# Performance work log

Measured on AMD Instinct MI355X. Metric: run time of the kernel, lower is better.

## Reference

```python
import jax, jax.numpy as jnp
import numpy as np

WIDTH = 1024
HEADS = 16
INIT_SCALE = 0.02


def setup_inputs() -> dict:
    key = jax.random.key(0)
    ks = jax.random.split(key, 5)
    x = jax.random.normal(ks[0], (2, 2048, WIDTH), dtype=jnp.float32)
    # torch Linear weight [out, in]; we store transposed [in, out] for x @ W
    W_qkv = jax.random.normal(ks[1], (WIDTH, 3 * WIDTH), dtype=jnp.float32) * INIT_SCALE
    b_qkv = jnp.zeros((3 * WIDTH,), dtype=jnp.float32)
    W_proj = jax.random.normal(ks[2], (WIDTH, WIDTH), dtype=jnp.float32) * INIT_SCALE
    b_proj = jnp.zeros((WIDTH,), dtype=jnp.float32)
    return {"x": x, "W_qkv": W_qkv, "b_qkv": b_qkv, "W_proj": W_proj, "b_proj": b_proj}


def reference(x, W_qkv, b_qkv, W_proj, b_proj):
    bs, n_ctx, width = x.shape
    heads = HEADS
    attn_ch = width // heads  # per-head channel dim (width*3 // heads // 3)
    scale = 1.0 / np.sqrt(np.sqrt(attn_ch))  # applied to both q and k

    qkv = x @ W_qkv + b_qkv                      # [b, t, 3*width]
    qkv = qkv.reshape(bs, n_ctx, heads, 3 * attn_ch)
    q, k, v = jnp.split(qkv, 3, axis=-1)         # each [b, t, h, c]

    weight = jnp.einsum('bthc,bshc->bhts', q * scale, k * scale)
    wdtype = weight.dtype
    weight = jax.nn.softmax(weight.astype(jnp.float32), axis=-1).astype(wdtype)

    out = jnp.einsum('bhts,bshc->bthc', weight, v).reshape(bs, n_ctx, width)
    return out @ W_proj + b_proj
```

## Files before the change

### kernel.cpp

```cpp
#include <hip/hip_runtime.h>

typedef __attribute__((ext_vector_type(4))) float fx4;
typedef __attribute__((ext_vector_type(16))) float f32x16;
typedef __attribute__((ext_vector_type(8))) short s16x8;
typedef __attribute__((ext_vector_type(2))) unsigned int u32x2;

#define QK_SCALE 0.35355339059327373f
#define LOG2E    1.4426950408889634f

__device__ __forceinline__ short f2bf(float f) {
  union { float f; unsigned int u; } v; v.f = f;
  unsigned int r = v.u + 0x7fffu + ((v.u >> 16) & 1u);
  return (short)(r >> 16);
}

__device__ __forceinline__ unsigned f2u(float f) {
  union { float f; unsigned u; } v; v.f = f; return v.u;
}
__device__ __forceinline__ float u2f(unsigned u) {
  union { unsigned u; float f; } v; v.u = u; return v.f;
}
__device__ __forceinline__ float bf2f(short s) {
  return u2f(((unsigned)(unsigned short)s) << 16);
}

__device__ __forceinline__ float xhalf_max(float x) {
  u32x2 r = __builtin_amdgcn_permlane32_swap(f2u(x), f2u(x), false, false);
  return fmaxf(u2f(r[0]), u2f(r[1]));
}
__device__ __forceinline__ float xhalf_sum(float x) {
  u32x2 r = __builtin_amdgcn_permlane32_swap(f2u(x), f2u(x), false, false);
  return u2f(r[0]) + u2f(r[1]);
}

__device__ __forceinline__ int swz(int row, int cb) {
  return (row * 128 + cb) ^ ((row & 7) << 4);
}

#define GLL(g, lds) __builtin_amdgcn_global_load_lds( \
    (__attribute__((address_space(1))) void*)(void*)(g), \
    (__attribute__((address_space(3))) void*)(void*)(lds), 16, 0, 0)

__global__ __launch_bounds__(256) void prep(
    const float* __restrict__ x, short* __restrict__ x16,
    const float* __restrict__ Wqkv, short* __restrict__ WqkvT,
    const float* __restrict__ Wproj, short* __restrict__ WprojT) {
  const int b = blockIdx.x;
  if (b < 4096) {
    int i = b * 256 + threadIdx.x;
    float4 v = reinterpret_cast<const float4*>(x)[i];
    short4 o;
    o.x = f2bf(v.x); o.y = f2bf(v.y); o.z = f2bf(v.z); o.w = f2bf(v.w);
    reinterpret_cast<short4*>(x16)[i] = o;
    return;
  }
  __shared__ float tile[32][33];
  const float* W; short* WT; int N, bx, by;
  if (b < 7168) { W = Wqkv; WT = WqkvT; N = 3072; int r = b - 4096; bx = r % 96; by = r / 96; }
  else          { W = Wproj; WT = WprojT; N = 1024; int r = b - 7168; bx = r % 32; by = r / 32; }
  const int K = 1024;
  int tx = threadIdx.x & 31, ty = threadIdx.x >> 5;
  int n0 = bx * 32, k0 = by * 32;
#pragma unroll
  for (int i = 0; i < 32; i += 8)
    tile[ty + i][tx] = W[(size_t)(k0 + ty + i) * N + n0 + tx];
  __syncthreads();
#pragma unroll
  for (int i = 0; i < 32; i += 8)
    WT[(size_t)(n0 + ty + i) * K + k0 + tx] = f2bf(tile[tx][ty + i]);
}

template <int MODE>
__global__ __launch_bounds__(256) void gemm_bf16(
    const short* __restrict__ A, const short* __restrict__ Bt,
    const float* __restrict__ bias, float* __restrict__ Cout,
    short* __restrict__ Qo, short* __restrict__ Ko, short* __restrict__ Vo,
    int M, int N, int K) {
  __shared__ __align__(16) char sA[2][128 * 64 * 2];
  __shared__ __align__(16) char sB[2][128 * 64 * 2];
  const int tid = threadIdx.x;
  const int w = tid >> 6, l = tid & 63;
  const int lr = l & 15, lg = l >> 4;
  const int bid = blockIdx.x;
  const int m0 = ((bid & 7) * 4 + ((bid >> 3) & 3)) * 128;
  const int n0 = (bid >> 5) * 128;
  const int wr = (w >> 1) * 64, wc = (w & 1) * 64;

  fx4 accT[4][4] = {};

#pragma unroll
  for (int i = 0; i < 4; ++i) {
    int c = i * 256 + tid;
    int r = c >> 3, p = c & 7;
    int lch = p ^ (r & 7);
    GLL(A + (size_t)(m0 + r) * K + lch * 8, sA[0] + c * 16);
    GLL(Bt + (size_t)(n0 + r) * K + lch * 8, sB[0] + c * 16);
  }
  __syncthreads();

  const int NIT = K >> 6;
  int cur = 0;
  for (int it = 0; it < NIT; ++it) {
    if (it + 1 < NIT) {
      int kt = (it + 1) * 64;
#pragma unroll
      for (int i = 0; i < 4; ++i) {
        int c = i * 256 + tid;
        int r = c >> 3, p = c & 7;
        int lch = p ^ (r & 7);
        GLL(A + (size_t)(m0 + r) * K + kt + lch * 8, sA[cur ^ 1] + c * 16);
        GLL(Bt + (size_t)(n0 + r) * K + kt + lch * 8, sB[cur ^ 1] + c * 16);
      }
    }
#pragma unroll
    for (int kk = 0; kk < 2; ++kk) {
      s16x8 av[4], bv[4];
#pragma unroll
      for (int m = 0; m < 4; ++m)
        av[m] = *reinterpret_cast<const s16x8*>(sA[cur] + swz(wr + m * 16 + lr, kk * 64 + lg * 16));
#pragma unroll
      for (int n = 0; n < 4; ++n)
        bv[n] = *reinterpret_cast<const s16x8*>(sB[cur] + swz(wc + n * 16 + lr, kk * 64 + lg * 16));
#pragma unroll
      for (int n = 0; n < 4; ++n)
#pragma unroll
        for (int m = 0; m < 4; ++m)
          accT[n][m] = __builtin_amdgcn_mfma_f32_16x16x32_bf16(bv[n], av[m], accT[n][m], 0, 0, 0);
    }
    __syncthreads();
    cur ^= 1;
  }

#pragma unroll
  for (int n = 0; n < 4; ++n) {
    const int col0 = n0 + wc + n * 16 + lg * 4;
    const float4 bs = *reinterpret_cast<const float4*>(bias + col0);
    if (MODE == 1) {
#pragma unroll
      for (int m = 0; m < 4; ++m) {
        int row = m0 + wr + m * 16 + lr;
        float4 v;
        v.x = accT[n][m][0] + bs.x; v.y = accT[n][m][1] + bs.y;
        v.z = accT[n][m][2] + bs.z; v.w = accT[n][m][3] + bs.w;
        *reinterpret_cast<float4*>(Cout + (size_t)row * N + col0) = v;
      }
    } else {
      const int h = col0 / 192;
      const int rr = col0 - h * 192;
#pragma unroll
      for (int m = 0; m < 4; ++m) {
        int row = m0 + wr + m * 16 + lr;
        int b = row >> 11, t = row & 2047;
        size_t bh = (size_t)b * 16 + h;
        float v0 = accT[n][m][0] + bs.x, v1 = accT[n][m][1] + bs.y;
        float v2 = accT[n][m][2] + bs.z, v3 = accT[n][m][3] + bs.w;
        if (rr < 64) {
          short4 s4;
          s4.x = f2bf(v0 * (QK_SCALE * LOG2E)); s4.y = f2bf(v1 * (QK_SCALE * LOG2E));
          s4.z = f2bf(v2 * (QK_SCALE * LOG2E)); s4.w = f2bf(v3 * (QK_SCALE * LOG2E));
          *reinterpret_cast<short4*>(Qo + (bh * 2048 + t) * 64 + rr) = s4;
        } else if (rr < 128) {
          short4 s4;
          s4.x = f2bf(v0 * QK_SCALE); s4.y = f2bf(v1 * QK_SCALE);
          s4.z = f2bf(v2 * QK_SCALE); s4.w = f2bf(v3 * QK_SCALE);
          *reinterpret_cast<short4*>(Ko + (bh * 2048 + t) * 64 + (rr - 64)) = s4;
        } else {
          Vo[(bh * 64 + (rr - 128) + 0) * 2048 + t] = f2bf(v0);
          Vo[(bh * 64 + (rr - 128) + 1) * 2048 + t] = f2bf(v1);
          Vo[(bh * 64 + (rr - 128) + 2) * 2048 + t] = f2bf(v2);
          Vo[(bh * 64 + (rr - 128) + 3) * 2048 + t] = f2bf(v3);
        }
      }
    }
  }
}

__global__ __launch_bounds__(256, 4) void attn_fwd(
    const short* __restrict__ Q, const short* __restrict__ Kc,
    const short* __restrict__ VT, short* __restrict__ OW,
    float2* __restrict__ ML) {
  __shared__ __align__(16) char sK[2][8192];
  __shared__ __align__(16) char sV[2][8192];
  const int tid = threadIdx.x;
  const int w = tid >> 6, l = tid & 63;
  const int l31 = l & 31, hi = l >> 5;
  const int bid = blockIdx.x;
  const int bh = (bid & 7) * 4 + ((bid >> 3) & 3);
  const int rest = bid >> 5;
  const int qt = rest >> 1, half = rest & 1;
  const int q0 = qt * 128 + w * 32;
  const int sbase = half * 1024;

  s16x8 qf[4];
  const short* qp = Q + ((size_t)bh * 2048 + q0 + l31) * 64 + hi * 8;
#pragma unroll
  for (int ks = 0; ks < 4; ++ks)
    qf[ks] = *reinterpret_cast<const s16x8*>(qp + ks * 16);

  float m = -1e30f, lsum = 0.f;
  f32x16 o0 = {}, o1 = {};

#pragma unroll
  for (int i = 0; i < 2; ++i) {
    int c = i * 256 + tid, r = c >> 3, pch = c & 7, lch = pch ^ (r & 7);
    GLL(Kc + ((size_t)bh * 2048 + sbase + r) * 64 + lch * 8, sK[0] + c * 16);
    GLL(VT + ((size_t)bh * 64 + r) * 2048 + sbase + lch * 8, sV[0] + c * 16);
  }
  __syncthreads();

  for (int sb = 0; sb < 16; ++sb) {
    const int s0 = sbase + sb * 64;
    if (sb < 15) {
#pragma unroll
      for (int i = 0; i < 2; ++i) {
        int c = i * 256 + tid, r = c >> 3, pch = c & 7, lch = pch ^ (r & 7);
        GLL(Kc + ((size_t)bh * 2048 + s0 + 64 + r) * 64 + lch * 8, sK[(sb + 1) & 1] + c * 16);
        GLL(VT + ((size_t)bh * 64 + r) * 2048 + s0 + 64 + lch * 8, sV[(sb + 1) & 1] + c * 16);
      }
    }
    const char* kb = sK[sb & 1];
    const char* vb = sV[sb & 1];

    f32x16 p0 = {}, p1 = {};
    __builtin_amdgcn_s_setprio(1);
#pragma unroll
    for (int ks = 0; ks < 4; ++ks) {
      int off = swz(l31, ks * 32 + hi * 16);
      s16x8 ka0 = *reinterpret_cast<const s16x8*>(kb + off);
      s16x8 ka1 = *reinterpret_cast<const s16x8*>(kb + off + 4096);
      p0 = __builtin_amdgcn_mfma_f32_32x32x16_bf16(ka0, qf[ks], p0, 0, 0, 0);
      p1 = __builtin_amdgcn_mfma_f32_32x32x16_bf16(ka1, qf[ks], p1, 0, 0, 0);
    }
    __builtin_amdgcn_s_setprio(0);

    float a8[8];
#pragma unroll
    for (int i = 0; i < 8; ++i)
      a8[i] = fmaxf(fmaxf(p0[2 * i], p0[2 * i + 1]), fmaxf(p1[2 * i], p1[2 * i + 1]));
    float pm = fmaxf(fmaxf(fmaxf(a8[0], a8[1]), fmaxf(a8[2], a8[3])),
                     fmaxf(fmaxf(a8[4], a8[5]), fmaxf(a8[6], a8[7])));
    pm = xhalf_max(pm);

    if (!__all(pm <= m + 11.5f)) {
      float mn = fmaxf(m, pm);
      float al = __builtin_amdgcn_exp2f(m - mn);
      m = mn;
      lsum *= al;
#pragma unroll
      for (int i = 0; i < 16; ++i) { o0[i] *= al; o1[i] *= al; }
    }
#pragma unroll
    for (int i = 0; i < 16; ++i) {
      p0[i] = __builtin_amdgcn_exp2f(p0[i] - m);
      p1[i] = __builtin_amdgcn_exp2f(p1[i] - m);
    }
    float s8[8];
#pragma unroll
    for (int i = 0; i < 8; ++i)
      s8[i] = (p0[2 * i] + p0[2 * i + 1]) + (p1[2 * i] + p1[2 * i + 1]);
    float rs = ((s8[0] + s8[1]) + (s8[2] + s8[3])) + ((s8[4] + s8[5]) + (s8[6] + s8[7]));
    lsum += xhalf_sum(rs);

    int wd[16];
#pragma unroll
    for (int i = 0; i < 8; ++i) {
      asm("v_cvt_pk_bf16_f32 %0, %1, %2" : "=v"(wd[i]) : "v"(p0[2 * i]), "v"(p0[2 * i + 1]));
      asm("v_cvt_pk_bf16_f32 %0, %1, %2" : "=v"(wd[8 + i]) : "v"(p1[2 * i]), "v"(p1[2 * i + 1]));
    }

    __builtin_amdgcn_s_setprio(1);
#pragma unroll
    for (int t = 0; t < 4; ++t) {
      u32x2 s02 = __builtin_amdgcn_permlane32_swap(
          (unsigned)wd[4 * t], (unsigned)wd[4 * t + 2], false, false);
      u32x2 s13 = __builtin_amdgcn_permlane32_swap(
          (unsigned)wd[4 * t + 1], (unsigned)wd[4 * t + 3], false, false);
      union { unsigned i4[4]; s16x8 v; } fr;
      fr.i4[0] = s02[0]; fr.i4[1] = s13[0]; fr.i4[2] = s02[1]; fr.i4[3] = s13[1];
      int off = swz(l31, t * 32 + hi * 16);
      s16x8 v0 = *reinterpret_cast<const s16x8*>(vb + off);
      s16x8 v1 = *reinterpret_cast<const s16x8*>(vb + off + 4096);
      o0 = __builtin_amdgcn_mfma_f32_32x32x16_bf16(v0, fr.v, o0, 0, 0, 0);
      o1 = __builtin_amdgcn_mfma_f32_32x32x16_bf16(v1, fr.v, o1, 0, 0, 0);
    }
    __builtin_amdgcn_s_setprio(0);
    __syncthreads();
  }

  short* owp = OW + (((size_t)(half * 32 + bh) * 2048) + q0 + l31) * 64 + hi * 4;
#pragma unroll
  for (int gq = 0; gq < 4; ++gq) {
    short4 s4;
    s4.x = f2bf(o0[4 * gq]);     s4.y = f2bf(o0[4 * gq + 1]);
    s4.z = f2bf(o0[4 * gq + 2]); s4.w = f2bf(o0[4 * gq + 3]);
    *reinterpret_cast<short4*>(owp + 8 * gq) = s4;
    s4.x = f2bf(o1[4 * gq]);     s4.y = f2bf(o1[4 * gq + 1]);
    s4.z = f2bf(o1[4 * gq + 2]); s4.w = f2bf(o1[4 * gq + 3]);
    *reinterpret_cast<short4*>(owp + 32 + 8 * gq) = s4;
  }
  if (hi == 0)
    ML[(size_t)(half * 32 + bh) * 2048 + q0 + l31] = make_float2(m, lsum);
}

__global__ __launch_bounds__(256) void attn_merge(
    const short* __restrict__ OW, const float2* __restrict__ ML,
    short* __restrict__ Y) {
  int gid = blockIdx.x * 256 + threadIdx.x;
  int row = gid >> 3, dc = (gid & 7) * 8;
  float2 ml0 = ML[row], ml1 = ML[65536 + row];
  float M = fmaxf(ml0.x, ml1.x);
  float w0 = __builtin_amdgcn_exp2f(ml0.x - M);
  float w1 = __builtin_amdgcn_exp2f(ml1.x - M);
  float inv = 1.f / (w0 * ml0.y + w1 * ml1.y);
  w0 *= inv; w1 *= inv;
  s16x8 a = *reinterpret_cast<const s16x8*>(OW + (size_t)row * 64 + dc);
  s16x8 bb = *reinterpret_cast<const s16x8*>(OW + (size_t)65536 * 64 + (size_t)row * 64 + dc);
  int bh = row >> 11, q = row & 2047;
  int b = bh >> 4, h = bh & 15;
  short* yp = Y + ((size_t)b * 2048 + q) * 1024 + h * 64 + dc;
  s16x8 o;
#pragma unroll
  for (int i = 0; i < 8; ++i)
    o[i] = f2bf(w0 * bf2f(a[i]) + w1 * bf2f(bb[i]));
  *reinterpret_cast<s16x8*>(yp) = o;
}

extern "C" void kernel_launch(void* const* d_in, const int* in_sizes, int n_in,
                              void* d_out, int out_size, void* d_ws, size_t ws_size,
                              hipStream_t stream) {
  const float* x     = (const float*)d_in[0];
  const float* Wqkv  = (const float*)d_in[1];
  const float* bqkv  = (const float*)d_in[2];
  const float* Wproj = (const float*)d_in[3];
  const float* bproj = (const float*)d_in[4];
  float* out = (float*)d_out;

  char* ws = (char*)d_ws;
  const size_t MB = 1024 * 1024;
  short* x16    = (short*)(ws);
  short* WqkvT  = (short*)(ws + 8 * MB);
  short* WprojT = (short*)(ws + 14 * MB);
  short* Q16    = (short*)(ws + 16 * MB);
  short* K16    = (short*)(ws + 24 * MB);
  short* VT16   = (short*)(ws + 32 * MB);
  short* OW     = (short*)(ws + 40 * MB);
  float2* ML    = (float2*)(ws + 58 * MB);
  short* Y16    = x16;

  prep<<<8192, 256, 0, stream>>>(x, x16, Wqkv, WqkvT, Wproj, WprojT);
  gemm_bf16<0><<<768, 256, 0, stream>>>(x16, WqkvT, bqkv, nullptr,
                                        Q16, K16, VT16, 4096, 3072, 1024);
  attn_fwd<<<1024, 256, 0, stream>>>(Q16, K16, VT16, OW, ML);
  attn_merge<<<2048, 256, 0, stream>>>(OW, ML, Y16);
  gemm_bf16<1><<<256, 256, 0, stream>>>(Y16, WprojT, bproj, out,
                                        nullptr, nullptr, nullptr, 4096, 1024, 1024);
}
```

Measured before the change: 130.8 us.

## Split attention keys into four chunks and drop LDS double buffering

The attention kernel now splits the key range four ways instead of two, doubling the grid to 2048 blocks with 8 key tiles each, and the merge kernel combines four partial outputs using their max/sum statistics. The K/V shared-memory double buffer is removed: each iteration loads a tile, syncs, then computes, which halves LDS use per block. The aim is more parallelism and occupancy. In exchange, loads no longer overlap compute, and there is extra partial-output traffic and merge work.

```diff
diff --git a/kernel.cpp b/kernel.cpp
--- a/kernel.cpp
+++ b/kernel.cpp
@@ -179,17 +179,17 @@
     const short* __restrict__ Q, const short* __restrict__ Kc,
     const short* __restrict__ VT, short* __restrict__ OW,
     float2* __restrict__ ML) {
-  __shared__ __align__(16) char sK[2][8192];
-  __shared__ __align__(16) char sV[2][8192];
+  __shared__ __align__(16) char sK[8192];
+  __shared__ __align__(16) char sV[8192];
   const int tid = threadIdx.x;
   const int w = tid >> 6, l = tid & 63;
   const int l31 = l & 31, hi = l >> 5;
   const int bid = blockIdx.x;
   const int bh = (bid & 7) * 4 + ((bid >> 3) & 3);
   const int rest = bid >> 5;
-  const int qt = rest >> 1, half = rest & 1;
+  const int qt = rest >> 2, quar = rest & 3;
   const int q0 = qt * 128 + w * 32;
-  const int sbase = half * 1024;
+  const int sbase = quar * 512;
 
   s16x8 qf[4];
   const short* qp = Q + ((size_t)bh * 2048 + q0 + l31) * 64 + hi * 8;
@@ -200,34 +200,23 @@
   float m = -1e30f, lsum = 0.f;
   f32x16 o0 = {}, o1 = {};
 
-#pragma unroll
-  for (int i = 0; i < 2; ++i) {
-    int c = i * 256 + tid, r = c >> 3, pch = c & 7, lch = pch ^ (r & 7);
-    GLL(Kc + ((size_t)bh * 2048 + sbase + r) * 64 + lch * 8, sK[0] + c * 16);
-    GLL(VT + ((size_t)bh * 64 + r) * 2048 + sbase + lch * 8, sV[0] + c * 16);
-  }
-  __syncthreads();
-
-  for (int sb = 0; sb < 16; ++sb) {
+  for (int sb = 0; sb < 8; ++sb) {
     const int s0 = sbase + sb * 64;
-    if (sb < 15) {
-#pragma unroll
-      for (int i = 0; i < 2; ++i) {
-        int c = i * 256 + tid, r = c >> 3, pch = c & 7, lch = pch ^ (r & 7);
-        GLL(Kc + ((size_t)bh * 2048 + s0 + 64 + r) * 64 + lch * 8, sK[(sb + 1) & 1] + c * 16);
-        GLL(VT + ((size_t)bh * 64 + r) * 2048 + s0 + 64 + lch * 8, sV[(sb + 1) & 1] + c * 16);
-      }
-    }
-    const char* kb = sK[sb & 1];
-    const char* vb = sV[sb & 1];
+#pragma unroll
+    for (int i = 0; i < 2; ++i) {
+      int c = i * 256 + tid, r = c >> 3, pch = c & 7, lch = pch ^ (r & 7);
+      GLL(Kc + ((size_t)bh * 2048 + s0 + r) * 64 + lch * 8, sK + c * 16);
+      GLL(VT + ((size_t)bh * 64 + r) * 2048 + s0 + lch * 8, sV + c * 16);
+    }
+    __syncthreads();
 
     f32x16 p0 = {}, p1 = {};
     __builtin_amdgcn_s_setprio(1);
 #pragma unroll
     for (int ks = 0; ks < 4; ++ks) {
       int off = swz(l31, ks * 32 + hi * 16);
-      s16x8 ka0 = *reinterpret_cast<const s16x8*>(kb + off);
-      s16x8 ka1 = *reinterpret_cast<const s16x8*>(kb + off + 4096);
+      s16x8 ka0 = *reinterpret_cast<const s16x8*>(sK + off);
+      s16x8 ka1 = *reinterpret_cast<const s16x8*>(sK + off + 4096);
       p0 = __builtin_amdgcn_mfma_f32_32x32x16_bf16(ka0, qf[ks], p0, 0, 0, 0);
       p1 = __builtin_amdgcn_mfma_f32_32x32x16_bf16(ka1, qf[ks], p1, 0, 0, 0);
     }
@@ -278,8 +267,8 @@
       union { unsigned i4[4]; s16x8 v; } fr;
       fr.i4[0] = s02[0]; fr.i4[1] = s13[0]; fr.i4[2] = s02[1]; fr.i4[3] = s13[1];
       int off = swz(l31, t * 32 + hi * 16);
-      s16x8 v0 = *reinterpret_cast<const s16x8*>(vb + off);
-      s16x8 v1 = *reinterpret_cast<const s16x8*>(vb + off + 4096);
+      s16x8 v0 = *reinterpret_cast<const s16x8*>(sV + off);
+      s16x8 v1 = *reinterpret_cast<const s16x8*>(sV + off + 4096);
       o0 = __builtin_amdgcn_mfma_f32_32x32x16_bf16(v0, fr.v, o0, 0, 0, 0);
       o1 = __builtin_amdgcn_mfma_f32_32x32x16_bf16(v1, fr.v, o1, 0, 0, 0);
     }
@@ -287,7 +276,7 @@
     __syncthreads();
   }
 
-  short* owp = OW + (((size_t)(half * 32 + bh) * 2048) + q0 + l31) * 64 + hi * 4;
+  short* owp = OW + (((size_t)(quar * 32 + bh) * 2048) + q0 + l31) * 64 + hi * 4;
 #pragma unroll
   for (int gq = 0; gq < 4; ++gq) {
     short4 s4;
@@ -299,7 +288,7 @@
     *reinterpret_cast<short4*>(owp + 32 + 8 * gq) = s4;
   }
   if (hi == 0)
-    ML[(size_t)(half * 32 + bh) * 2048 + q0 + l31] = make_float2(m, lsum);
+    ML[(size_t)(quar * 32 + bh) * 2048 + q0 + l31] = make_float2(m, lsum);
 }
 
 __global__ __launch_bounds__(256) void attn_merge(
@@ -307,21 +296,31 @@
     short* __restrict__ Y) {
   int gid = blockIdx.x * 256 + threadIdx.x;
   int row = gid >> 3, dc = (gid & 7) * 8;
-  float2 ml0 = ML[row], ml1 = ML[65536 + row];
-  float M = fmaxf(ml0.x, ml1.x);
+  float2 ml0 = ML[row];
+  float2 ml1 = ML[65536 + row];
+  float2 ml2 = ML[131072 + row];
+  float2 ml3 = ML[196608 + row];
+  float M = fmaxf(fmaxf(ml0.x, ml1.x), fmaxf(ml2.x, ml3.x));
   float w0 = __builtin_amdgcn_exp2f(ml0.x - M);
   float w1 = __builtin_amdgcn_exp2f(ml1.x - M);
-  float inv = 1.f / (w0 * ml0.y + w1 * ml1.y);
-  w0 *= inv; w1 *= inv;
-  s16x8 a = *reinterpret_cast<const s16x8*>(OW + (size_t)row * 64 + dc);
-  s16x8 bb = *reinterpret_cast<const s16x8*>(OW + (size_t)65536 * 64 + (size_t)row * 64 + dc);
+  float w2 = __builtin_amdgcn_exp2f(ml2.x - M);
+  float w3 = __builtin_amdgcn_exp2f(ml3.x - M);
+  float inv = 1.f / (w0 * ml0.y + w1 * ml1.y + w2 * ml2.y + w3 * ml3.y);
+  w0 *= inv; w1 *= inv; w2 *= inv; w3 *= inv;
+  const size_t stride = (size_t)65536 * 64;
+  size_t base = (size_t)row * 64 + dc;
+  s16x8 a0 = *reinterpret_cast<const s16x8*>(OW + base);
+  s16x8 a1 = *reinterpret_cast<const s16x8*>(OW + stride + base);
+  s16x8 a2 = *reinterpret_cast<const s16x8*>(OW + 2 * stride + base);
+  s16x8 a3 = *reinterpret_cast<const s16x8*>(OW + 3 * stride + base);
   int bh = row >> 11, q = row & 2047;
   int b = bh >> 4, h = bh & 15;
   short* yp = Y + ((size_t)b * 2048 + q) * 1024 + h * 64 + dc;
   s16x8 o;
 #pragma unroll
   for (int i = 0; i < 8; ++i)
-    o[i] = f2bf(w0 * bf2f(a[i]) + w1 * bf2f(bb[i]));
+    o[i] = f2bf(w0 * bf2f(a0[i]) + w1 * bf2f(a1[i]) +
+                w2 * bf2f(a2[i]) + w3 * bf2f(a3[i]));
   *reinterpret_cast<s16x8*>(yp) = o;
 }
 
@@ -344,13 +343,13 @@
   short* K16    = (short*)(ws + 24 * MB);
   short* VT16   = (short*)(ws + 32 * MB);
   short* OW     = (short*)(ws + 40 * MB);
-  float2* ML    = (float2*)(ws + 58 * MB);
+  float2* ML    = (float2*)(ws + 74 * MB);
   short* Y16    = x16;
 
   prep<<<8192, 256, 0, stream>>>(x, x16, Wqkv, WqkvT, Wproj, WprojT);
   gemm_bf16<0><<<768, 256, 0, stream>>>(x16, WqkvT, bqkv, nullptr,
                                         Q16, K16, VT16, 4096, 3072, 1024);
-  attn_fwd<<<1024, 256, 0, stream>>>(Q16, K16, VT16, OW, ML);
+  attn_fwd<<<2048, 256, 0, stream>>>(Q16, K16, VT16, OW, ML);
   attn_merge<<<2048, 256, 0, stream>>>(OW, ML, Y16);
   gemm_bf16<1><<<256, 256, 0, stream>>>(Y16, WprojT, bproj, out,
                                         nullptr, nullptr, nullptr, 4096, 1024, 1024);
```

After: 133.8 us. 2.3% more time.
